# Kernel optimization log

Measured on AMD Instinct MI355X. Metric: run time of the kernel, lower is better.

The kernel has to match this reference:

```python
import jax, jax.numpy as jnp
import numpy as np

K = 3          # kernel_size (local window)
PAD = 1        # padding = (K-1)//2 -> 'same' output size
GROUPS = 8
C_OUT = 64


def _unfold3d(x, k):
    """x: [B,C,Dp,Hp,Wp] -> [B,C,D,H,W,kd,kh,kw] sliding windows (stride 1)."""
    B, C, Dp, Hp, Wp = x.shape
    D, H, W = Dp - k + 1, Hp - k + 1, Wp - k + 1
    idx_d = jnp.arange(D)[:, None] + jnp.arange(k)[None, :]
    idx_h = jnp.arange(H)[:, None] + jnp.arange(k)[None, :]
    idx_w = jnp.arange(W)[:, None] + jnp.arange(k)[None, :]
    x = x[:, :, idx_d]              # [B,C,D,kd,Hp,Wp]
    x = x[:, :, :, :, idx_h]        # [B,C,D,kd,H,kh,Wp]
    x = x[:, :, :, :, :, :, idx_w]  # [B,C,D,kd,H,kh,W,kw]
    return jnp.transpose(x, (0, 1, 2, 4, 6, 3, 5, 7))


def setup_inputs() -> dict:
    key = jax.random.key(0)
    ks = jax.random.split(key, 7)
    B, Cin, D, H, W = 1, 64, 16, 64, 64
    c3 = C_OUT // 3                 # 21
    rest = C_OUT - 2 * c3           # 22
    fan_out_scale = np.sqrt(2.0 / C_OUT)  # kaiming_normal fan_out, relu
    x = jax.random.normal(ks[0], (B, Cin, D, H, W), dtype=jnp.float32)
    w_q = jax.random.normal(ks[1], (C_OUT, Cin), dtype=jnp.float32) * fan_out_scale
    w_k = jax.random.normal(ks[2], (C_OUT, Cin), dtype=jnp.float32) * fan_out_scale
    w_v = jax.random.normal(ks[3], (C_OUT, Cin), dtype=jnp.float32) * fan_out_scale
    rel_d = jax.random.normal(ks[4], (c3, 1, 1, 1, K, 1, 1), dtype=jnp.float32)
    rel_h = jax.random.normal(ks[5], (c3, 1, 1, 1, 1, K, 1), dtype=jnp.float32)
    rel_w = jax.random.normal(ks[6], (rest, 1, 1, 1, 1, 1, K), dtype=jnp.float32)
    return {"x": x, "w_q": w_q, "w_k": w_k, "w_v": w_v,
            "rel_d": rel_d, "rel_h": rel_h, "rel_w": rel_w}


def reference(x, w_q, w_k, w_v, rel_d, rel_h, rel_w):
    B, Cin, D, H, W = x.shape
    cg = C_OUT // GROUPS
    c3 = C_OUT // 3
    # 1x1x1 convs (bias=False): plain channel mixing. conv(pad(x)) == pad(conv(x)).
    q = jnp.einsum('oc,bcdhw->bodhw', w_q, x)
    k = jnp.einsum('oc,bcdhw->bodhw', w_k, x)
    v = jnp.einsum('oc,bcdhw->bodhw', w_v, x)
    pad = [(0, 0), (0, 0), (PAD, PAD), (PAD, PAD), (PAD, PAD)]
    k = jnp.pad(k, pad)
    v = jnp.pad(v, pad)
    k_win = _unfold3d(k, K)   # [B,Co,D,H,W,kd,kh,kw]
    v_win = _unfold3d(v, K)
    # split relative position bias across channel thirds
    k_win = jnp.concatenate([
        k_win[:, :c3] + rel_d,
        k_win[:, c3:2 * c3] + rel_h,
        k_win[:, 2 * c3:] + rel_w,
    ], axis=1)
    Kv = K * K * K
    k_win = k_win.reshape(B, GROUPS, cg, D, H, W, Kv)
    v_win = v_win.reshape(B, GROUPS, cg, D, H, W, Kv)
    qg = q.reshape(B, GROUPS, cg, D, H, W, 1)
    attn = jax.nn.softmax(qg * k_win, axis=-1)
    out = jnp.einsum('bncdhwk,bncdhwk->bncdhw', attn, v_win)
    return out.reshape(B, C_OUT, D, H, W)
```

## Files before the change

kernel.cpp:

```cpp
#include <hip/hip_runtime.h>

#define SP    65536
#define DD    16
#define HH    64
#define WW    64
#define CIN   64
#define COUT  64

#define LOG2E 1.44269504f


typedef __attribute__((ext_vector_type(8))) short bf16x8;
typedef __attribute__((ext_vector_type(4))) float f32x4;

__device__ __forceinline__ unsigned short f2bf(float f) {
    const unsigned u = __float_as_uint(f);
    return (unsigned short)((u + 0x7FFFu + ((u >> 16) & 1u)) >> 16);
}
__device__ __forceinline__ float bf2f(unsigned short h) {
    return __uint_as_float((unsigned)h << 16);
}

__global__ __launch_bounds__(256) void proj(const float* __restrict__ x,
                                            const float* __restrict__ wq,
                                            const float* __restrict__ wk,
                                            const float* __restrict__ wv,
                                            float* __restrict__ q,
                                            float* __restrict__ k,
                                            float* __restrict__ v) {
    __shared__ __align__(16) unsigned short xh [64][72];
    __shared__ __align__(16) unsigned short xlo[64][72];
    __shared__ __align__(16) unsigned short wh [64][72];
    __shared__ __align__(16) unsigned short wlo[64][72];

    const int t  = threadIdx.x;
    const int p0 = blockIdx.x * 64;
    const int m  = blockIdx.y;

    const float* __restrict__ wsel = (m == 0) ? wq : (m == 1) ? wk : wv;
    float* __restrict__       osel = (m == 0) ? q  : (m == 1) ? k  : v;

#pragma unroll
    for (int i = 0; i < 2; ++i) {
        const int f  = t + 256 * i;
        const int c2 = (f >> 4) * 2;
        const int jj = f & 15;
        const float4 a = *(const float4*)(x + c2 * SP + p0 + jj * 4);
        const float4 b = *(const float4*)(x + (c2 + 1) * SP + p0 + jj * 4);
        const float* af = (const float*)&a;
        const float* bf = (const float*)&b;
#pragma unroll
        for (int e = 0; e < 4; ++e) {
            const int j = jj * 4 + e;
            const unsigned short ah = f2bf(af[e]);
            const unsigned short bh = f2bf(bf[e]);
            const unsigned short al = f2bf(af[e] - bf2f(ah));
            const unsigned short bl = f2bf(bf[e] - bf2f(bh));
            *(unsigned*)&xh [j][c2] = (unsigned)ah | ((unsigned)bh << 16);
            *(unsigned*)&xlo[j][c2] = (unsigned)al | ((unsigned)bl << 16);
        }
    }
#pragma unroll
    for (int i = 0; i < 4; ++i) {
        const int f  = t + 256 * i;
        const int o  = f >> 4;
        const int jj = f & 15;
        const float4 w4 = *(const float4*)(wsel + o * CIN + jj * 4);
        const float* wf = (const float*)&w4;
        unsigned short h0 = f2bf(wf[0]), h1 = f2bf(wf[1]);
        unsigned short h2 = f2bf(wf[2]), h3 = f2bf(wf[3]);
        unsigned short l0 = f2bf(wf[0] - bf2f(h0)), l1 = f2bf(wf[1] - bf2f(h1));
        unsigned short l2 = f2bf(wf[2] - bf2f(h2)), l3 = f2bf(wf[3] - bf2f(h3));
        *(uint2*)&wh [o][jj * 4] = make_uint2((unsigned)h0 | ((unsigned)h1 << 16),
                                              (unsigned)h2 | ((unsigned)h3 << 16));
        *(uint2*)&wlo[o][jj * 4] = make_uint2((unsigned)l0 | ((unsigned)l1 << 16),
                                              (unsigned)l2 | ((unsigned)l3 << 16));
    }
    __syncthreads();

    const int lane  = t & 63;
    const int wid   = t >> 6;
    const int lo16  = lane & 15;
    const int lg    = lane >> 4;
    const int otile = wid * 16;

    const bf16x8 Ah0 = *(const bf16x8*)&wh [otile + lo16][lg * 8];
    const bf16x8 Ah1 = *(const bf16x8*)&wh [otile + lo16][32 + lg * 8];
    const bf16x8 Al0 = *(const bf16x8*)&wlo[otile + lo16][lg * 8];
    const bf16x8 Al1 = *(const bf16x8*)&wlo[otile + lo16][32 + lg * 8];

    const float scale = (m == 0) ? LOG2E : 1.f;

#pragma unroll
    for (int jt = 0; jt < 4; ++jt) {
        const int jr = jt * 16 + lo16;
        const bf16x8 Bh0 = *(const bf16x8*)&xh [jr][lg * 8];
        const bf16x8 Bl0 = *(const bf16x8*)&xlo[jr][lg * 8];
        const bf16x8 Bh1 = *(const bf16x8*)&xh [jr][32 + lg * 8];
        const bf16x8 Bl1 = *(const bf16x8*)&xlo[jr][32 + lg * 8];
        f32x4 hh = {0.f, 0.f, 0.f, 0.f};
        f32x4 hl = {0.f, 0.f, 0.f, 0.f};
        f32x4 lh = {0.f, 0.f, 0.f, 0.f};
        hh = __builtin_amdgcn_mfma_f32_16x16x32_bf16(Ah0, Bh0, hh, 0, 0, 0);
        hl = __builtin_amdgcn_mfma_f32_16x16x32_bf16(Ah0, Bl0, hl, 0, 0, 0);
        lh = __builtin_amdgcn_mfma_f32_16x16x32_bf16(Al0, Bh0, lh, 0, 0, 0);
        hh = __builtin_amdgcn_mfma_f32_16x16x32_bf16(Ah1, Bh1, hh, 0, 0, 0);
        hl = __builtin_amdgcn_mfma_f32_16x16x32_bf16(Ah1, Bl1, hl, 0, 0, 0);
        lh = __builtin_amdgcn_mfma_f32_16x16x32_bf16(Al1, Bh1, lh, 0, 0, 0);
        float* op = osel + (otile + lg * 4) * SP + p0 + jt * 16 + lo16;
#pragma unroll
        for (int r = 0; r < 4; ++r)
            op[r * SP] = (hh[r] + hl[r] + lh[r]) * scale;
    }
}

__device__ __forceinline__ float dpp_shr1(float x) {
    return __int_as_float(__builtin_amdgcn_mov_dpp(__float_as_int(x), 0x111, 0xf, 0xf, true));
}
__device__ __forceinline__ float dpp_shl1(float x) {
    return __int_as_float(__builtin_amdgcn_mov_dpp(__float_as_int(x), 0x101, 0xf, 0xf, true));
}

template<int AXIS>
__device__ __forceinline__ void attn_tile(const float* __restrict__ kt,
                                          const float* __restrict__ vt,
                                          const float (&ql)[2][4],
                                          float r0, float r1, float r2,
                                          int wg, int h, int dg,
                                          float (&s)[2][4], float (&a)[2][4]) {
#pragma unroll
    for (int nl = 0; nl < 4; ++nl) {
#pragma unroll
        for (int kh = 0; kh < 3; ++kh) {
            const int off = ((dg * 2 + nl) * 10 + h + kh) * 64 + wg * 4;
            const float4 km = *(const float4*)(kt + off);
            const float4 vm = *(const float4*)(vt + off);
            const float kl = dpp_shr1(km.w), kr = dpp_shl1(km.x);
            const float vl = dpp_shr1(vm.w), vr = dpp_shl1(vm.x);
            const float krow[6] = { kl, km.x, km.y, km.z, km.w, kr };
            const float vrow[6] = { vl, vm.x, vm.y, vm.z, vm.w, vr };

            const float rkh = (kh == 0) ? r0 : (kh == 1) ? r1 : r2;

#pragma unroll
            for (int di = 0; di < 2; ++di) {
                const int kd = nl - di;
                if (kd >= 0 && kd < 3) {
                    const float rdd = (kd == 0) ? r0 : (kd == 1) ? r1 : r2;
                    const float rr  = (AXIS == 0) ? rdd : (AXIS == 1) ? rkh : 0.f;
#pragma unroll
                    for (int wi = 0; wi < 4; ++wi) {
                        const float qv = ql[di][wi];
#pragma unroll
                        for (int kw = 0; kw < 3; ++kw) {
                            const float rc = (AXIS == 2)
                                           ? ((kw == 0) ? r0 : (kw == 1) ? r1 : r2)
                                           : rr;
                            const float e = __builtin_amdgcn_exp2f(qv * (krow[wi + kw] + rc));
                            s[di][wi] += e;
                            a[di][wi] = fmaf(e, vrow[wi + kw], a[di][wi]);
                        }
                    }
                }
            }
        }
    }
}

__global__ __launch_bounds__(256) void attn(const float* __restrict__ kbuf,
                                            const float* __restrict__ vbuf,
                                            const float* __restrict__ qbuf,
                                            const float* __restrict__ rel_d,
                                            const float* __restrict__ rel_h,
                                            const float* __restrict__ rel_w,
                                            float* __restrict__ out) {
    __shared__ float kt[60 * 64];
    __shared__ float vt[60 * 64];

    const int dt = blockIdx.x;
    const int ht = blockIdx.y;
    const int o  = blockIdx.z;

    const int d0 = dt * 4;
    const int h0 = ht * 8;
    const int t  = threadIdx.x;

    const float* __restrict__ kc = kbuf + o * SP;
    const float* __restrict__ vc = vbuf + o * SP;

#pragma unroll
    for (int i = 0; i < 8; ++i) {
        const int idx = t + 256 * i;
        if (idx < 1920) {
            const bool isv = idx >= 960;
            const int rem  = isv ? idx - 960 : idx;
            const int row  = rem >> 4;
            const int j    = rem & 15;
            const int nn   = row / 10;
            const int hp   = row - nn * 10;
            const int dpg  = d0 - 1 + nn;
            const int hpg  = h0 - 1 + hp;
            float4 val = make_float4(0.f, 0.f, 0.f, 0.f);
            if ((unsigned)dpg < (unsigned)DD && (unsigned)hpg < (unsigned)HH) {
                const float* src = (isv ? vc : kc) + (dpg * HH + hpg) * WW + j * 4;
                val = *(const float4*)src;
            }
            *(float4*)((isv ? vt : kt) + row * 64 + j * 4) = val;
        }
    }

    const int wg = t & 15;
    const int h  = (t >> 4) & 7;
    const int dg = t >> 7;

    float ql[2][4];
#pragma unroll
    for (int di = 0; di < 2; ++di) {
        const int dabs = d0 + dg * 2 + di;
        const float4 q4 = *(const float4*)(qbuf + o * SP + (dabs * HH + (h0 + h)) * WW + wg * 4);
        ql[di][0] = q4.x; ql[di][1] = q4.y;
        ql[di][2] = q4.z; ql[di][3] = q4.w;
    }

    __syncthreads();

    float s[2][4] = {};
    float a[2][4] = {};

    if (o < 21) {
        attn_tile<0>(kt, vt, ql, rel_d[o * 3 + 0], rel_d[o * 3 + 1], rel_d[o * 3 + 2],
                     wg, h, dg, s, a);
    } else if (o < 42) {
        const int b = o - 21;
        attn_tile<1>(kt, vt, ql, rel_h[b * 3 + 0], rel_h[b * 3 + 1], rel_h[b * 3 + 2],
                     wg, h, dg, s, a);
    } else {
        const int b = o - 42;
        attn_tile<2>(kt, vt, ql, rel_w[b * 3 + 0], rel_w[b * 3 + 1], rel_w[b * 3 + 2],
                     wg, h, dg, s, a);
    }

#pragma unroll
    for (int di = 0; di < 2; ++di) {
        const int dabs = d0 + dg * 2 + di;
        float4 ov;
        ov.x = a[di][0] * __builtin_amdgcn_rcpf(s[di][0]);
        ov.y = a[di][1] * __builtin_amdgcn_rcpf(s[di][1]);
        ov.z = a[di][2] * __builtin_amdgcn_rcpf(s[di][2]);
        ov.w = a[di][3] * __builtin_amdgcn_rcpf(s[di][3]);
        *(float4*)(out + o * SP + (dabs * HH + (h0 + h)) * WW + wg * 4) = ov;
    }
}

extern "C" void kernel_launch(void* const* d_in, const int* in_sizes, int n_in,
                              void* d_out, int out_size, void* d_ws, size_t ws_size,
                              hipStream_t stream) {
    const float* x     = (const float*)d_in[0];
    const float* w_q   = (const float*)d_in[1];
    const float* w_k   = (const float*)d_in[2];
    const float* w_v   = (const float*)d_in[3];
    const float* rel_d = (const float*)d_in[4];
    const float* rel_h = (const float*)d_in[5];
    const float* rel_w = (const float*)d_in[6];
    float* out = (float*)d_out;

    float* ws = (float*)d_ws;
    float* q  = ws;
    float* k  = ws + (size_t)COUT * SP;
    float* v  = ws + 2 * (size_t)COUT * SP;

    proj<<<dim3(SP / 64, 3), 256, 0, stream>>>(x, w_q, w_k, w_v, q, k, v);
    attn<<<dim3(4, 8, 64), 256, 0, stream>>>(k, v, q, rel_d, rel_h, rel_w, out);
}
```

Measured before the change: 119.5 us.

## Read K/V windows directly from global memory instead of LDS staging

Removes the shared-memory tiles for K and V and the cooperative load plus barrier. Each thread now loads its float4 rows straight from global memory (relying on L1/L2 for reuse across neighbouring threads), with bounds checks for padding. It also adds a minimum-occupancy hint of 5 blocks per CU to launch_bounds. This trades the LDS traffic and sync for more global/cache loads, 24 per thread inside the compute loop, which may expose latency.

After: 266.5 us. +122.9%, slower.

```diff
diff --git a/kernel.cpp b/kernel.cpp
--- a/kernel.cpp
+++ b/kernel.cpp
@@ -122,19 +122,27 @@
 }
 
 template<int AXIS>
-__device__ __forceinline__ void attn_tile(const float* __restrict__ kt,
-                                          const float* __restrict__ vt,
+__device__ __forceinline__ void attn_tile(const float* __restrict__ kc,
+                                          const float* __restrict__ vc,
                                           const float (&ql)[2][4],
                                           float r0, float r1, float r2,
-                                          int wg, int h, int dg,
+                                          int wg, int h, int d0, int h0, int dg,
                                           float (&s)[2][4], float (&a)[2][4]) {
 #pragma unroll
     for (int nl = 0; nl < 4; ++nl) {
+        const int dpg = d0 - 1 + dg * 2 + nl;
 #pragma unroll
         for (int kh = 0; kh < 3; ++kh) {
-            const int off = ((dg * 2 + nl) * 10 + h + kh) * 64 + wg * 4;
-            const float4 km = *(const float4*)(kt + off);
-            const float4 vm = *(const float4*)(vt + off);
+            const int hpg = h0 - 1 + h + kh;
+            const bool ok = ((unsigned)dpg < (unsigned)DD) &&
+                            ((unsigned)hpg < (unsigned)HH);
+            const int off = ok ? ((dpg * HH + hpg) * WW + wg * 4) : 0;
+            float4 km = *(const float4*)(kc + off);
+            float4 vm = *(const float4*)(vc + off);
+            if (!ok) {
+                km = make_float4(0.f, 0.f, 0.f, 0.f);
+                vm = make_float4(0.f, 0.f, 0.f, 0.f);
+            }
             const float kl = dpp_shr1(km.w), kr = dpp_shl1(km.x);
             const float vl = dpp_shr1(vm.w), vr = dpp_shl1(vm.x);
             const float krow[6] = { kl, km.x, km.y, km.z, km.w, kr };
@@ -167,16 +175,13 @@
     }
 }
 
-__global__ __launch_bounds__(256) void attn(const float* __restrict__ kbuf,
-                                            const float* __restrict__ vbuf,
-                                            const float* __restrict__ qbuf,
-                                            const float* __restrict__ rel_d,
-                                            const float* __restrict__ rel_h,
-                                            const float* __restrict__ rel_w,
-                                            float* __restrict__ out) {
-    __shared__ float kt[60 * 64];
-    __shared__ float vt[60 * 64];
-
+__global__ __launch_bounds__(256, 5) void attn(const float* __restrict__ kbuf,
+                                               const float* __restrict__ vbuf,
+                                               const float* __restrict__ qbuf,
+                                               const float* __restrict__ rel_d,
+                                               const float* __restrict__ rel_h,
+                                               const float* __restrict__ rel_w,
+                                               float* __restrict__ out) {
     const int dt = blockIdx.x;
     const int ht = blockIdx.y;
     const int o  = blockIdx.z;
@@ -187,27 +192,6 @@
 
     const float* __restrict__ kc = kbuf + o * SP;
     const float* __restrict__ vc = vbuf + o * SP;
-
-#pragma unroll
-    for (int i = 0; i < 8; ++i) {
-        const int idx = t + 256 * i;
-        if (idx < 1920) {
-            const bool isv = idx >= 960;
-            const int rem  = isv ? idx - 960 : idx;
-            const int row  = rem >> 4;
-            const int j    = rem & 15;
-            const int nn   = row / 10;
-            const int hp   = row - nn * 10;
-            const int dpg  = d0 - 1 + nn;
-            const int hpg  = h0 - 1 + hp;
-            float4 val = make_float4(0.f, 0.f, 0.f, 0.f);
-            if ((unsigned)dpg < (unsigned)DD && (unsigned)hpg < (unsigned)HH) {
-                const float* src = (isv ? vc : kc) + (dpg * HH + hpg) * WW + j * 4;
-                val = *(const float4*)src;
-            }
-            *(float4*)((isv ? vt : kt) + row * 64 + j * 4) = val;
-        }
-    }
 
     const int wg = t & 15;
     const int h  = (t >> 4) & 7;
@@ -222,22 +206,20 @@
         ql[di][2] = q4.z; ql[di][3] = q4.w;
     }
 
-    __syncthreads();
-
     float s[2][4] = {};
     float a[2][4] = {};
 
     if (o < 21) {
-        attn_tile<0>(kt, vt, ql, rel_d[o * 3 + 0], rel_d[o * 3 + 1], rel_d[o * 3 + 2],
-                     wg, h, dg, s, a);
+        attn_tile<0>(kc, vc, ql, rel_d[o * 3 + 0], rel_d[o * 3 + 1], rel_d[o * 3 + 2],
+                     wg, h, d0, h0, dg, s, a);
     } else if (o < 42) {
         const int b = o - 21;
-        attn_tile<1>(kt, vt, ql, rel_h[b * 3 + 0], rel_h[b * 3 + 1], rel_h[b * 3 + 2],
-                     wg, h, dg, s, a);
+        attn_tile<1>(kc, vc, ql, rel_h[b * 3 + 0], rel_h[b * 3 + 1], rel_h[b * 3 + 2],
+                     wg, h, d0, h0, dg, s, a);
     } else {
         const int b = o - 42;
-        attn_tile<2>(kt, vt, ql, rel_w[b * 3 + 0], rel_w[b * 3 + 1], rel_w[b * 3 + 2],
-                     wg, h, dg, s, a);
+        attn_tile<2>(kc, vc, ql, rel_w[b * 3 + 0], rel_w[b * 3 + 1], rel_w[b * 3 + 2],
+                     wg, h, d0, h0, dg, s, a);
     }
 
 #pragma unroll
```

## Compute Q/K/V in one projection block and replace axis templates with bias table

Applied to the files above, without the earlier changes.

The projection kernel now handles all three weight matrices per block. Each x tile is loaded and split into bf16 hi/lo once instead of three times, and the weights are loaded straight from global memory into registers rather than staged through shared memory. The attention kernel drops its three template instantiations. It builds a 27-entry relative-bias table made wave-uniform with readfirstlane, so every block runs a single code path. This costs more registers in proj and adds a per-element table lookup in place of compile-time-selected bias values.

Result: slower. 144.7 us (+21.1%).

```diff
diff --git a/kernel.cpp b/kernel.cpp
--- a/kernel.cpp
+++ b/kernel.cpp
@@ -30,15 +30,9 @@
                                             float* __restrict__ v) {
     __shared__ __align__(16) unsigned short xh [64][72];
     __shared__ __align__(16) unsigned short xlo[64][72];
-    __shared__ __align__(16) unsigned short wh [64][72];
-    __shared__ __align__(16) unsigned short wlo[64][72];
 
     const int t  = threadIdx.x;
     const int p0 = blockIdx.x * 64;
-    const int m  = blockIdx.y;
-
-    const float* __restrict__ wsel = (m == 0) ? wq : (m == 1) ? wk : wv;
-    float* __restrict__       osel = (m == 0) ? q  : (m == 1) ? k  : v;
 
 #pragma unroll
     for (int i = 0; i < 2; ++i) {
@@ -60,23 +54,6 @@
             *(unsigned*)&xlo[j][c2] = (unsigned)al | ((unsigned)bl << 16);
         }
     }
-#pragma unroll
-    for (int i = 0; i < 4; ++i) {
-        const int f  = t + 256 * i;
-        const int o  = f >> 4;
-        const int jj = f & 15;
-        const float4 w4 = *(const float4*)(wsel + o * CIN + jj * 4);
-        const float* wf = (const float*)&w4;
-        unsigned short h0 = f2bf(wf[0]), h1 = f2bf(wf[1]);
-        unsigned short h2 = f2bf(wf[2]), h3 = f2bf(wf[3]);
-        unsigned short l0 = f2bf(wf[0] - bf2f(h0)), l1 = f2bf(wf[1] - bf2f(h1));
-        unsigned short l2 = f2bf(wf[2] - bf2f(h2)), l3 = f2bf(wf[3] - bf2f(h3));
-        *(uint2*)&wh [o][jj * 4] = make_uint2((unsigned)h0 | ((unsigned)h1 << 16),
-                                              (unsigned)h2 | ((unsigned)h3 << 16));
-        *(uint2*)&wlo[o][jj * 4] = make_uint2((unsigned)l0 | ((unsigned)l1 << 16),
-                                              (unsigned)l2 | ((unsigned)l3 << 16));
-    }
-    __syncthreads();
 
     const int lane  = t & 63;
     const int wid   = t >> 6;
@@ -84,12 +61,33 @@
     const int lg    = lane >> 4;
     const int otile = wid * 16;
 
-    const bf16x8 Ah0 = *(const bf16x8*)&wh [otile + lo16][lg * 8];
-    const bf16x8 Ah1 = *(const bf16x8*)&wh [otile + lo16][32 + lg * 8];
-    const bf16x8 Al0 = *(const bf16x8*)&wlo[otile + lo16][lg * 8];
-    const bf16x8 Al1 = *(const bf16x8*)&wlo[otile + lo16][32 + lg * 8];
-
-    const float scale = (m == 0) ? LOG2E : 1.f;
+    const float* wptr[3] = { wq, wk, wv };
+    bf16x8 Ah[3][2], Al[3][2];
+#pragma unroll
+    for (int m = 0; m < 3; ++m) {
+#pragma unroll
+        for (int ch = 0; ch < 2; ++ch) {
+            const float* src = wptr[m] + (otile + lo16) * CIN + ch * 32 + lg * 8;
+            const float4 f0 = *(const float4*)src;
+            const float4 f1 = *(const float4*)(src + 4);
+            float fv[8];
+            *(float4*)&fv[0] = f0;
+            *(float4*)&fv[4] = f1;
+            bf16x8 hv, lv;
+#pragma unroll
+            for (int e = 0; e < 8; ++e) {
+                const unsigned short hb = f2bf(fv[e]);
+                hv[e] = (short)hb;
+                lv[e] = (short)f2bf(fv[e] - bf2f(hb));
+            }
+            Ah[m][ch] = hv;
+            Al[m][ch] = lv;
+        }
+    }
+    __syncthreads();
+
+    float* outp[3] = { q, k, v };
+    const float scl[3] = { LOG2E, 1.f, 1.f };
 
 #pragma unroll
     for (int jt = 0; jt < 4; ++jt) {
@@ -98,19 +96,22 @@
         const bf16x8 Bl0 = *(const bf16x8*)&xlo[jr][lg * 8];
         const bf16x8 Bh1 = *(const bf16x8*)&xh [jr][32 + lg * 8];
         const bf16x8 Bl1 = *(const bf16x8*)&xlo[jr][32 + lg * 8];
-        f32x4 hh = {0.f, 0.f, 0.f, 0.f};
-        f32x4 hl = {0.f, 0.f, 0.f, 0.f};
-        f32x4 lh = {0.f, 0.f, 0.f, 0.f};
-        hh = __builtin_amdgcn_mfma_f32_16x16x32_bf16(Ah0, Bh0, hh, 0, 0, 0);
-        hl = __builtin_amdgcn_mfma_f32_16x16x32_bf16(Ah0, Bl0, hl, 0, 0, 0);
-        lh = __builtin_amdgcn_mfma_f32_16x16x32_bf16(Al0, Bh0, lh, 0, 0, 0);
-        hh = __builtin_amdgcn_mfma_f32_16x16x32_bf16(Ah1, Bh1, hh, 0, 0, 0);
-        hl = __builtin_amdgcn_mfma_f32_16x16x32_bf16(Ah1, Bl1, hl, 0, 0, 0);
-        lh = __builtin_amdgcn_mfma_f32_16x16x32_bf16(Al1, Bh1, lh, 0, 0, 0);
-        float* op = osel + (otile + lg * 4) * SP + p0 + jt * 16 + lo16;
-#pragma unroll
-        for (int r = 0; r < 4; ++r)
-            op[r * SP] = (hh[r] + hl[r] + lh[r]) * scale;
+#pragma unroll
+        for (int m = 0; m < 3; ++m) {
+            f32x4 hh = {0.f, 0.f, 0.f, 0.f};
+            f32x4 hl = {0.f, 0.f, 0.f, 0.f};
+            f32x4 lh = {0.f, 0.f, 0.f, 0.f};
+            hh = __builtin_amdgcn_mfma_f32_16x16x32_bf16(Ah[m][0], Bh0, hh, 0, 0, 0);
+            hl = __builtin_amdgcn_mfma_f32_16x16x32_bf16(Ah[m][0], Bl0, hl, 0, 0, 0);
+            lh = __builtin_amdgcn_mfma_f32_16x16x32_bf16(Al[m][0], Bh0, lh, 0, 0, 0);
+            hh = __builtin_amdgcn_mfma_f32_16x16x32_bf16(Ah[m][1], Bh1, hh, 0, 0, 0);
+            hl = __builtin_amdgcn_mfma_f32_16x16x32_bf16(Ah[m][1], Bl1, hl, 0, 0, 0);
+            lh = __builtin_amdgcn_mfma_f32_16x16x32_bf16(Al[m][1], Bh1, lh, 0, 0, 0);
+            float* op = outp[m] + (otile + lg * 4) * SP + p0 + jt * 16 + lo16;
+#pragma unroll
+            for (int r = 0; r < 4; ++r)
+                op[r * SP] = (hh[r] + hl[r] + lh[r]) * scl[m];
+        }
     }
 }
 
@@ -121,11 +122,10 @@
     return __int_as_float(__builtin_amdgcn_mov_dpp(__float_as_int(x), 0x101, 0xf, 0xf, true));
 }
 
-template<int AXIS>
 __device__ __forceinline__ void attn_tile(const float* __restrict__ kt,
                                           const float* __restrict__ vt,
                                           const float (&ql)[2][4],
-                                          float r0, float r1, float r2,
+                                          const float (&R)[27],
                                           int wg, int h, int dg,
                                           float (&s)[2][4], float (&a)[2][4]) {
 #pragma unroll
@@ -140,22 +140,16 @@
             const float krow[6] = { kl, km.x, km.y, km.z, km.w, kr };
             const float vrow[6] = { vl, vm.x, vm.y, vm.z, vm.w, vr };
 
-            const float rkh = (kh == 0) ? r0 : (kh == 1) ? r1 : r2;
-
 #pragma unroll
             for (int di = 0; di < 2; ++di) {
                 const int kd = nl - di;
                 if (kd >= 0 && kd < 3) {
-                    const float rdd = (kd == 0) ? r0 : (kd == 1) ? r1 : r2;
-                    const float rr  = (AXIS == 0) ? rdd : (AXIS == 1) ? rkh : 0.f;
 #pragma unroll
                     for (int wi = 0; wi < 4; ++wi) {
                         const float qv = ql[di][wi];
 #pragma unroll
                         for (int kw = 0; kw < 3; ++kw) {
-                            const float rc = (AXIS == 2)
-                                           ? ((kw == 0) ? r0 : (kw == 1) ? r1 : r2)
-                                           : rr;
+                            const float rc = R[kd * 9 + kh * 3 + kw];
                             const float e = __builtin_amdgcn_exp2f(qv * (krow[wi + kw] + rc));
                             s[di][wi] += e;
                             a[di][wi] = fmaf(e, vrow[wi + kw], a[di][wi]);
@@ -209,6 +203,28 @@
         }
     }
 
+    float ra0, ra1, ra2;
+    int ax;
+    if (o < 21)      { ax = 0; ra0 = rel_d[o * 3]; ra1 = rel_d[o * 3 + 1]; ra2 = rel_d[o * 3 + 2]; }
+    else if (o < 42) { ax = 1; const int b = o - 21;
+                       ra0 = rel_h[b * 3]; ra1 = rel_h[b * 3 + 1]; ra2 = rel_h[b * 3 + 2]; }
+    else             { ax = 2; const int b = o - 42;
+                       ra0 = rel_w[b * 3]; ra1 = rel_w[b * 3 + 1]; ra2 = rel_w[b * 3 + 2]; }
+    float R[27];
+#pragma unroll
+    for (int kd = 0; kd < 3; ++kd)
+#pragma unroll
+        for (int kh = 0; kh < 3; ++kh)
+#pragma unroll
+            for (int kw = 0; kw < 3; ++kw) {
+                const float vd = (kd == 0) ? ra0 : (kd == 1) ? ra1 : ra2;
+                const float vh = (kh == 0) ? ra0 : (kh == 1) ? ra1 : ra2;
+                const float vw = (kw == 0) ? ra0 : (kw == 1) ? ra1 : ra2;
+                const float rv = (ax == 0) ? vd : (ax == 1) ? vh : vw;
+                R[kd * 9 + kh * 3 + kw] =
+                    __uint_as_float(__builtin_amdgcn_readfirstlane(__float_as_uint(rv)));
+            }
+
     const int wg = t & 15;
     const int h  = (t >> 4) & 7;
     const int dg = t >> 7;
@@ -226,19 +242,7 @@
 
     float s[2][4] = {};
     float a[2][4] = {};
-
-    if (o < 21) {
-        attn_tile<0>(kt, vt, ql, rel_d[o * 3 + 0], rel_d[o * 3 + 1], rel_d[o * 3 + 2],
-                     wg, h, dg, s, a);
-    } else if (o < 42) {
-        const int b = o - 21;
-        attn_tile<1>(kt, vt, ql, rel_h[b * 3 + 0], rel_h[b * 3 + 1], rel_h[b * 3 + 2],
-                     wg, h, dg, s, a);
-    } else {
-        const int b = o - 42;
-        attn_tile<2>(kt, vt, ql, rel_w[b * 3 + 0], rel_w[b * 3 + 1], rel_w[b * 3 + 2],
-                     wg, h, dg, s, a);
-    }
+    attn_tile(kt, vt, ql, R, wg, h, dg, s, a);
 
 #pragma unroll
     for (int di = 0; di < 2; ++di) {
@@ -269,6 +273,6 @@
     float* k  = ws + (size_t)COUT * SP;
     float* v  = ws + 2 * (size_t)COUT * SP;
 
-    proj<<<dim3(SP / 64, 3), 256, 0, stream>>>(x, w_q, w_k, w_v, q, k, v);
+    proj<<<dim3(SP / 64), 256, 0, stream>>>(x, w_q, w_k, w_v, q, k, v);
     attn<<<dim3(4, 8, 64), 256, 0, stream>>>(k, v, q, rel_d, rel_h, rel_w, out);
 }
```

## Shrink attention tile to one output row per thread with table-driven bias

Applied to the files above, without the earlier changes.

The attention kernel now gives each thread a single output depth row instead of two, with 4x4 d/h tiles per block. The launch doubles the block count, and the shared-memory halo shrinks from 60 to 36 rows per tensor. The three axis-specialised template paths collapse into one loop that reads a 27-entry wave-uniform bias table built with readfirstlane, and launch bounds ask for 6 blocks per CU. The aim is more occupancy and less divergent code, paid for with a larger halo-to-interior load ratio (each K/V row is reused across fewer outputs) and more blocks to schedule.

Measured after the change: 222.8 us. +86.4%, slower.

```diff
diff --git a/kernel.cpp b/kernel.cpp
--- a/kernel.cpp
+++ b/kernel.cpp
@@ -121,85 +121,39 @@
     return __int_as_float(__builtin_amdgcn_mov_dpp(__float_as_int(x), 0x101, 0xf, 0xf, true));
 }
 
-template<int AXIS>
-__device__ __forceinline__ void attn_tile(const float* __restrict__ kt,
-                                          const float* __restrict__ vt,
-                                          const float (&ql)[2][4],
-                                          float r0, float r1, float r2,
-                                          int wg, int h, int dg,
-                                          float (&s)[2][4], float (&a)[2][4]) {
-#pragma unroll
-    for (int nl = 0; nl < 4; ++nl) {
-#pragma unroll
-        for (int kh = 0; kh < 3; ++kh) {
-            const int off = ((dg * 2 + nl) * 10 + h + kh) * 64 + wg * 4;
-            const float4 km = *(const float4*)(kt + off);
-            const float4 vm = *(const float4*)(vt + off);
-            const float kl = dpp_shr1(km.w), kr = dpp_shl1(km.x);
-            const float vl = dpp_shr1(vm.w), vr = dpp_shl1(vm.x);
-            const float krow[6] = { kl, km.x, km.y, km.z, km.w, kr };
-            const float vrow[6] = { vl, vm.x, vm.y, vm.z, vm.w, vr };
-
-            const float rkh = (kh == 0) ? r0 : (kh == 1) ? r1 : r2;
-
-#pragma unroll
-            for (int di = 0; di < 2; ++di) {
-                const int kd = nl - di;
-                if (kd >= 0 && kd < 3) {
-                    const float rdd = (kd == 0) ? r0 : (kd == 1) ? r1 : r2;
-                    const float rr  = (AXIS == 0) ? rdd : (AXIS == 1) ? rkh : 0.f;
-#pragma unroll
-                    for (int wi = 0; wi < 4; ++wi) {
-                        const float qv = ql[di][wi];
-#pragma unroll
-                        for (int kw = 0; kw < 3; ++kw) {
-                            const float rc = (AXIS == 2)
-                                           ? ((kw == 0) ? r0 : (kw == 1) ? r1 : r2)
-                                           : rr;
-                            const float e = __builtin_amdgcn_exp2f(qv * (krow[wi + kw] + rc));
-                            s[di][wi] += e;
-                            a[di][wi] = fmaf(e, vrow[wi + kw], a[di][wi]);
-                        }
-                    }
-                }
-            }
-        }
-    }
-}
-
-__global__ __launch_bounds__(256) void attn(const float* __restrict__ kbuf,
-                                            const float* __restrict__ vbuf,
-                                            const float* __restrict__ qbuf,
-                                            const float* __restrict__ rel_d,
-                                            const float* __restrict__ rel_h,
-                                            const float* __restrict__ rel_w,
-                                            float* __restrict__ out) {
-    __shared__ float kt[60 * 64];
-    __shared__ float vt[60 * 64];
+__global__ __launch_bounds__(256, 6) void attn(const float* __restrict__ kbuf,
+                                               const float* __restrict__ vbuf,
+                                               const float* __restrict__ qbuf,
+                                               const float* __restrict__ rel_d,
+                                               const float* __restrict__ rel_h,
+                                               const float* __restrict__ rel_w,
+                                               float* __restrict__ out) {
+    __shared__ float kt[36 * 64];
+    __shared__ float vt[36 * 64];
 
     const int dt = blockIdx.x;
     const int ht = blockIdx.y;
     const int o  = blockIdx.z;
 
     const int d0 = dt * 4;
-    const int h0 = ht * 8;
+    const int h0 = ht * 4;
     const int t  = threadIdx.x;
 
     const float* __restrict__ kc = kbuf + o * SP;
     const float* __restrict__ vc = vbuf + o * SP;
 
 #pragma unroll
-    for (int i = 0; i < 8; ++i) {
+    for (int i = 0; i < 5; ++i) {
         const int idx = t + 256 * i;
-        if (idx < 1920) {
-            const bool isv = idx >= 960;
-            const int rem  = isv ? idx - 960 : idx;
+        if (idx < 1152) {
+            const bool isv = idx >= 576;
+            const int rem  = isv ? idx - 576 : idx;
             const int row  = rem >> 4;
             const int j    = rem & 15;
-            const int nn   = row / 10;
-            const int hp   = row - nn * 10;
-            const int dpg  = d0 - 1 + nn;
-            const int hpg  = h0 - 1 + hp;
+            const int nd   = row / 6;
+            const int nh   = row - nd * 6;
+            const int dpg  = d0 - 1 + nd;
+            const int hpg  = h0 - 1 + nh;
             float4 val = make_float4(0.f, 0.f, 0.f, 0.f);
             if ((unsigned)dpg < (unsigned)DD && (unsigned)hpg < (unsigned)HH) {
                 const float* src = (isv ? vc : kc) + (dpg * HH + hpg) * WW + j * 4;
@@ -209,47 +163,78 @@
         }
     }
 
+    float ra0, ra1, ra2;
+    int ax;
+    if (o < 21)      { ax = 0; ra0 = rel_d[o * 3]; ra1 = rel_d[o * 3 + 1]; ra2 = rel_d[o * 3 + 2]; }
+    else if (o < 42) { ax = 1; const int b = o - 21;
+                       ra0 = rel_h[b * 3]; ra1 = rel_h[b * 3 + 1]; ra2 = rel_h[b * 3 + 2]; }
+    else             { ax = 2; const int b = o - 42;
+                       ra0 = rel_w[b * 3]; ra1 = rel_w[b * 3 + 1]; ra2 = rel_w[b * 3 + 2]; }
+    float R[27];
+#pragma unroll
+    for (int kd = 0; kd < 3; ++kd)
+#pragma unroll
+        for (int kh = 0; kh < 3; ++kh)
+#pragma unroll
+            for (int kw = 0; kw < 3; ++kw) {
+                const float vd = (kd == 0) ? ra0 : (kd == 1) ? ra1 : ra2;
+                const float vh = (kh == 0) ? ra0 : (kh == 1) ? ra1 : ra2;
+                const float vw = (kw == 0) ? ra0 : (kw == 1) ? ra1 : ra2;
+                const float rv = (ax == 0) ? vd : (ax == 1) ? vh : vw;
+                R[kd * 9 + kh * 3 + kw] =
+                    __uint_as_float(__builtin_amdgcn_readfirstlane(__float_as_uint(rv)));
+            }
+
     const int wg = t & 15;
-    const int h  = (t >> 4) & 7;
-    const int dg = t >> 7;
-
-    float ql[2][4];
-#pragma unroll
-    for (int di = 0; di < 2; ++di) {
-        const int dabs = d0 + dg * 2 + di;
-        const float4 q4 = *(const float4*)(qbuf + o * SP + (dabs * HH + (h0 + h)) * WW + wg * 4);
-        ql[di][0] = q4.x; ql[di][1] = q4.y;
-        ql[di][2] = q4.z; ql[di][3] = q4.w;
+    const int hl = (t >> 4) & 3;
+    const int dl = t >> 6;
+
+    const int dabs = d0 + dl;
+    const int habs = h0 + hl;
+
+    float ql[4];
+    {
+        const float4 q4 = *(const float4*)(qbuf + o * SP + (dabs * HH + habs) * WW + wg * 4);
+        ql[0] = q4.x; ql[1] = q4.y;
+        ql[2] = q4.z; ql[3] = q4.w;
     }
 
     __syncthreads();
 
-    float s[2][4] = {};
-    float a[2][4] = {};
-
-    if (o < 21) {
-        attn_tile<0>(kt, vt, ql, rel_d[o * 3 + 0], rel_d[o * 3 + 1], rel_d[o * 3 + 2],
-                     wg, h, dg, s, a);
-    } else if (o < 42) {
-        const int b = o - 21;
-        attn_tile<1>(kt, vt, ql, rel_h[b * 3 + 0], rel_h[b * 3 + 1], rel_h[b * 3 + 2],
-                     wg, h, dg, s, a);
-    } else {
-        const int b = o - 42;
-        attn_tile<2>(kt, vt, ql, rel_w[b * 3 + 0], rel_w[b * 3 + 1], rel_w[b * 3 + 2],
-                     wg, h, dg, s, a);
-    }
-
-#pragma unroll
-    for (int di = 0; di < 2; ++di) {
-        const int dabs = d0 + dg * 2 + di;
-        float4 ov;
-        ov.x = a[di][0] * __builtin_amdgcn_rcpf(s[di][0]);
-        ov.y = a[di][1] * __builtin_amdgcn_rcpf(s[di][1]);
-        ov.z = a[di][2] * __builtin_amdgcn_rcpf(s[di][2]);
-        ov.w = a[di][3] * __builtin_amdgcn_rcpf(s[di][3]);
-        *(float4*)(out + o * SP + (dabs * HH + (h0 + h)) * WW + wg * 4) = ov;
-    }
+    float s[4] = {};
+    float a[4] = {};
+
+#pragma unroll
+    for (int kd = 0; kd < 3; ++kd) {
+#pragma unroll
+        for (int kh = 0; kh < 3; ++kh) {
+            const int off = ((dl + kd) * 6 + hl + kh) * 64 + wg * 4;
+            const float4 km = *(const float4*)(kt + off);
+            const float4 vm = *(const float4*)(vt + off);
+            const float kl = dpp_shr1(km.w), kr = dpp_shl1(km.x);
+            const float vl = dpp_shr1(vm.w), vr = dpp_shl1(vm.x);
+            const float krow[6] = { kl, km.x, km.y, km.z, km.w, kr };
+            const float vrow[6] = { vl, vm.x, vm.y, vm.z, vm.w, vr };
+#pragma unroll
+            for (int wi = 0; wi < 4; ++wi) {
+                const float qv = ql[wi];
+#pragma unroll
+                for (int kw = 0; kw < 3; ++kw) {
+                    const float rc = R[kd * 9 + kh * 3 + kw];
+                    const float e = __builtin_amdgcn_exp2f(qv * (krow[wi + kw] + rc));
+                    s[wi] += e;
+                    a[wi] = fmaf(e, vrow[wi + kw], a[wi]);
+                }
+            }
+        }
+    }
+
+    float4 ov;
+    ov.x = a[0] * __builtin_amdgcn_rcpf(s[0]);
+    ov.y = a[1] * __builtin_amdgcn_rcpf(s[1]);
+    ov.z = a[2] * __builtin_amdgcn_rcpf(s[2]);
+    ov.w = a[3] * __builtin_amdgcn_rcpf(s[3]);
+    *(float4*)(out + o * SP + (dabs * HH + habs) * WW + wg * 4) = ov;
 }
 
 extern "C" void kernel_launch(void* const* d_in, const int* in_sizes, int n_in,
@@ -270,5 +255,5 @@
     float* v  = ws + 2 * (size_t)COUT * SP;
 
     proj<<<dim3(SP / 64, 3), 256, 0, stream>>>(x, w_q, w_k, w_v, q, k, v);
-    attn<<<dim3(4, 8, 64), 256, 0, stream>>>(k, v, q, rel_d, rel_h, rel_w, out);
-}
+    attn<<<dim3(4, 16, 64), 256, 0, stream>>>(k, v, q, rel_d, rel_h, rel_w, out);
+}
```
